# Performance work log

Hardware: AMD Instinct MI355X
Metric: run time of the kernel (lower is better)

## Reference

```python
import jax, jax.numpy as jnp
import numpy as np

N = 50000
E_RAND = 800000
F_IN = 128
H = 4          # num_heads
D_HID = 32     # hidden per-head dim
D_OUT = 32     # output per-head dim
NEG_SLOPE_ATTN = 0.2   # DGL GATConv attention leaky_relu
NEG_SLOPE_ACT = 0.01   # F.leaky_relu default activation


def setup_inputs() -> dict:
    key = jax.random.key(0)
    ks = jax.random.split(key, 12)
    x = jax.random.normal(ks[0], (N, F_IN), dtype=jnp.float32)
    src_r = jax.random.randint(ks[1], (E_RAND,), 0, N, dtype=jnp.int32)
    dst_r = jax.random.randint(ks[2], (E_RAND,), 0, N, dtype=jnp.int32)
    loop = jnp.arange(N, dtype=jnp.int32)
    src = jnp.concatenate([src_r, loop])  # add_self_loop
    dst = jnp.concatenate([dst_r, loop])
    sc1 = 1.0 / np.sqrt(F_IN)
    sc2 = 1.0 / np.sqrt(H * D_HID)
    W1 = jax.random.normal(ks[3], (F_IN, H * D_HID), dtype=jnp.float32) * sc1
    al1 = jax.random.normal(ks[4], (H, D_HID), dtype=jnp.float32) * sc1
    ar1 = jax.random.normal(ks[5], (H, D_HID), dtype=jnp.float32) * sc1
    b1 = jnp.zeros((H * D_HID,), dtype=jnp.float32)
    W2 = jax.random.normal(ks[6], (H * D_HID, H * D_OUT), dtype=jnp.float32) * sc2
    al2 = jax.random.normal(ks[7], (H, D_OUT), dtype=jnp.float32) * sc2
    ar2 = jax.random.normal(ks[8], (H, D_OUT), dtype=jnp.float32) * sc2
    b2 = jnp.zeros((H * D_OUT,), dtype=jnp.float32)
    return {"x": x, "src": src, "dst": dst,
            "W1": W1, "al1": al1, "ar1": ar1, "b1": b1,
            "W2": W2, "al2": al2, "ar2": ar2, "b2": b2}


def gat_conv(x, src, dst, W, al, ar, b, act_slope):
    n = x.shape[0]
    h, d = al.shape
    feat = (x @ W).reshape(n, h, d)                 # [N,H,D]
    el = jnp.einsum('nhd,hd->nh', feat, al)         # [N,H]
    er = jnp.einsum('nhd,hd->nh', feat, ar)
    # edge attention score on edge u->v: leaky_relu(el[u] + er[v])
    e = jax.nn.leaky_relu(el[src] + er[dst], NEG_SLOPE_ATTN)  # [E,H]
    # edge softmax over incoming edges of each dst node (self-loops guarantee >=1 edge)
    m = jax.ops.segment_max(e, dst, num_segments=n)           # [N,H]
    ex = jnp.exp(e - m[dst])
    s = jax.ops.segment_sum(ex, dst, num_segments=n)
    a = ex / s[dst]                                           # [E,H]
    # attention-weighted scatter-sum of source features
    out = jax.ops.segment_sum(a[:, :, None] * feat[src], dst, num_segments=n)  # [N,H,D]
    out = out + b.reshape(h, d)
    if act_slope is not None:
        out = jax.nn.leaky_relu(out, act_slope)
    return out.reshape(n, h * d)                    # flatten(1)


def reference(x, src, dst, W1, al1, ar1, b1, W2, al2, ar2, b2):
    h = gat_conv(x, src, dst, W1, al1, ar1, b1, NEG_SLOPE_ACT)
    out = gat_conv(h, src, dst, W2, al2, ar2, b2, None)  # last layer: no activation
    return out
```

## Files before the change

### kernel.cpp

```cpp
#include <hip/hip_runtime.h>
#include <hip/hip_bf16.h>
#include <hip/hip_fp16.h>

#define HEADS 4
#define DHEAD 32
#define FDIM 128
#define BCAP 64

__global__ __launch_bounds__(256) void k_gemm(
    const float* __restrict__ X, const float* __restrict__ W,
    const float* __restrict__ al, const float* __restrict__ ar,
    __half* __restrict__ feat, float* __restrict__ el, float* __restrict__ er, int n,
    const int* __restrict__ esrc, const int* __restrict__ edst,
    int* __restrict__ deg, int* __restrict__ bucket, int E) {
    __shared__ float Wl[FDIM * FDIM];
    {
        const float4* W4 = (const float4*)W;
        float4* Wl4 = (float4*)Wl;
        for (int i = threadIdx.x; i < FDIM * FDIM / 4; i += 256) Wl4[i] = W4[i];
    }

    if (E > 0) {
        int nb = gridDim.x;
        int echunk = (E + nb - 1) / nb;
        int e0 = blockIdx.x * echunk;
        int e1 = e0 + echunk; if (e1 > E) e1 = E;
        for (int base = e0 + threadIdx.x; base < e1; base += 256 * 8) {
            int d[8], s[8];
#pragma unroll
            for (int j = 0; j < 8; j++) {
                int idx = base + j * 256;
                if (idx < e1) { d[j] = edst[idx]; s[j] = esrc[idx]; }
                else d[j] = -1;
            }
#pragma unroll
            for (int j = 0; j < 8; j++) {
                if (d[j] >= 0) {
                    int p = atomicAdd(&deg[d[j]], 1);
                    if (p < BCAP) bucket[((size_t)d[j] << 6) + p] = s[j];
                }
            }
        }
    }
    __syncthreads();

    int h = __builtin_amdgcn_readfirstlane(threadIdx.x >> 6);
    int lane = threadIdx.x & 63;
    int rb = blockIdx.x * 256 + lane * 4;

    bool v[4];
    const float4* xp[4];
#pragma unroll
    for (int i = 0; i < 4; i++) {
        v[i] = (rb + i) < n;
        int cr = v[i] ? (rb + i) : (n - 1);
        xp[i] = (const float4*)(X + (size_t)cr * FDIM);
    }

    float acc[4][32];
#pragma unroll
    for (int i = 0; i < 4; i++)
#pragma unroll
        for (int j = 0; j < 32; j++) acc[i][j] = 0.f;

    const float* wbase = Wl + h * DHEAD;

    for (int k4 = 0; k4 < FDIM / 4; k4++) {
        float4 a[4];
#pragma unroll
        for (int i = 0; i < 4; i++) a[i] = xp[i][k4];
#pragma unroll
        for (int kk = 0; kk < 4; kk++) {
            const float4* wr = (const float4*)(wbase + (k4 * 4 + kk) * FDIM);
            float s[4];
#pragma unroll
            for (int i = 0; i < 4; i++) s[i] = (&a[i].x)[kk];
#pragma unroll
            for (int j4 = 0; j4 < 8; j4++) {
                float4 wv = wr[j4];
#pragma unroll
                for (int i = 0; i < 4; i++) {
                    acc[i][j4*4+0] += s[i] * wv.x;
                    acc[i][j4*4+1] += s[i] * wv.y;
                    acc[i][j4*4+2] += s[i] * wv.z;
                    acc[i][j4*4+3] += s[i] * wv.w;
                }
            }
        }
    }

    float elv[4], erv[4];
#pragma unroll
    for (int i = 0; i < 4; i++) { elv[i] = 0.f; erv[i] = 0.f; }
#pragma unroll
    for (int j = 0; j < 32; j++) {
        float va = al[h * DHEAD + j], vr = ar[h * DHEAD + j];
#pragma unroll
        for (int i = 0; i < 4; i++) {
            elv[i] += acc[i][j] * va;
            erv[i] += acc[i][j] * vr;
        }
    }
#pragma unroll
    for (int i = 0; i < 4; i++) {
        if (v[i]) {
            el[(size_t)(rb + i) * HEADS + h] = elv[i];
            er[(size_t)(rb + i) * HEADS + h] = erv[i];
        }
    }

#pragma unroll
    for (int i = 0; i < 4; i++) {
        if (!v[i]) continue;
        union { __half2 h2[16]; uint4 u4[4]; } pk;
#pragma unroll
        for (int m = 0; m < 16; m++)
            pk.h2[m] = __floats2half2_rn(acc[i][2*m], acc[i][2*m+1]);
        uint4* dstp = (uint4*)(feat + (size_t)(rb + i) * FDIM + h * DHEAD);
#pragma unroll
        for (int t = 0; t < 4; t++) dstp[t] = pk.u4[t];
    }
}

__global__ __launch_bounds__(256) void k_aggregate(
    const int* __restrict__ bucket, const int* __restrict__ deg,
    const __half2* __restrict__ feat2h, const float* __restrict__ el,
    const float* __restrict__ er, const float* __restrict__ b,
    float* __restrict__ out, int n, int apply_act) {
    int wave = threadIdx.x >> 6;
    int node = blockIdx.x * 4 + wave;
    if (node >= n) return;
    node = __builtin_amdgcn_readfirstlane(node);
    int lane = threadIdx.x & 63;
    int h = lane >> 4;

    float ern = er[(size_t)node * HEADS + h];
    int cnt = __builtin_amdgcn_readfirstlane(deg[node]);
    const int* bkt = bucket + ((size_t)node << 6);

    float ax = 0.f, ay = 0.f, sw = 0.f;
    int i = 0;

    for (; i + 8 <= cnt; i += 8) {
        int s[8];
#pragma unroll
        for (int j = 0; j < 8; j++) s[j] = bkt[i + j];
        float e[8];
#pragma unroll
        for (int j = 0; j < 8; j++) e[j] = el[(size_t)s[j] * HEADS + h];
        __half2 f[8];
#pragma unroll
        for (int j = 0; j < 8; j++) f[j] = feat2h[(size_t)s[j] * 64 + lane];
#pragma unroll
        for (int j = 0; j < 8; j++) {
            float ev = e[j] + ern;
            ev = ev > 0.f ? ev : 0.2f * ev;
            float w = __expf(ev);
            float2 fv = __half22float2(f[j]);
            sw += w; ax += w * fv.x; ay += w * fv.y;
        }
    }
    for (; i + 2 <= cnt; i += 2) {
        int s0 = bkt[i], s1 = bkt[i + 1];
        float e0 = el[(size_t)s0 * HEADS + h];
        float e1 = el[(size_t)s1 * HEADS + h];
        __half2 f0 = feat2h[(size_t)s0 * 64 + lane];
        __half2 f1 = feat2h[(size_t)s1 * 64 + lane];
        e0 += ern; e0 = e0 > 0.f ? e0 : 0.2f * e0;
        e1 += ern; e1 = e1 > 0.f ? e1 : 0.2f * e1;
        float w0 = __expf(e0), w1 = __expf(e1);
        float2 fv0 = __half22float2(f0), fv1 = __half22float2(f1);
        sw += w0 + w1;
        ax += w0 * fv0.x + w1 * fv1.x;
        ay += w0 * fv0.y + w1 * fv1.y;
    }
    if (i < cnt) {
        int s0 = bkt[i];
        float e0 = el[(size_t)s0 * HEADS + h] + ern;
        e0 = e0 > 0.f ? e0 : 0.2f * e0;
        float w0 = __expf(e0);
        float2 fv0 = __half22float2(feat2h[(size_t)s0 * 64 + lane]);
        sw += w0; ax += w0 * fv0.x; ay += w0 * fv0.y;
    }

    float inv = 1.0f / sw;
    float2 bv = ((const float2*)b)[lane];
    float ox = ax * inv + bv.x;
    float oy = ay * inv + bv.y;
    if (apply_act) {
        ox = ox > 0.f ? ox : 0.01f * ox;
        oy = oy > 0.f ? oy : 0.01f * oy;
    }
    float2 o; o.x = ox; o.y = oy;
    ((float2*)out)[(size_t)node * 64 + lane] = o;
}


extern "C" void kernel_launch(void* const* d_in, const int* in_sizes, int n_in,
                              void* d_out, int out_size, void* d_ws, size_t ws_size,
                              hipStream_t stream) {
    const float* x   = (const float*)d_in[0];
    const int*   src = (const int*)d_in[1];
    const int*   dst = (const int*)d_in[2];
    const float* W1  = (const float*)d_in[3];
    const float* al1 = (const float*)d_in[4];
    const float* ar1 = (const float*)d_in[5];
    const float* b1  = (const float*)d_in[6];
    const float* W2  = (const float*)d_in[7];
    const float* al2 = (const float*)d_in[8];
    const float* ar2 = (const float*)d_in[9];
    const float* b2  = (const float*)d_in[10];
    int N = in_sizes[0] / FDIM;
    int E = in_sizes[1];
    float* out = (float*)d_out;

    __half* featA = (__half*)d_ws;
    float* elb    = (float*)(featA + (size_t)N * FDIM);
    float* erb    = elb + (size_t)N * HEADS;
    int*   deg    = (int*)(erb + (size_t)N * HEADS);
    int*   bucket = deg + N;
    float* hbuf   = out;

    int gblocks = (N + 255) / 256;

    hipMemsetAsync(deg, 0, (size_t)N * sizeof(int), stream);

    k_gemm<<<gblocks, 256, 0, stream>>>(x, W1, al1, ar1, featA, elb, erb, N,
                                        src, dst, deg, bucket, E);
    k_aggregate<<<(N + 3) / 4, 256, 0, stream>>>(bucket, deg, (const __half2*)featA,
                                                 elb, erb, b1, hbuf, N, 1);

    k_gemm<<<gblocks, 256, 0, stream>>>(hbuf, W2, al2, ar2, featA, elb, erb, N,
                                        nullptr, nullptr, nullptr, nullptr, 0);
    k_aggregate<<<(N + 3) / 4, 256, 0, stream>>>(bucket, deg, (const __half2*)featA,
                                                 elb, erb, b2, out, N, 0);
}
```

Baseline: 274.6 us.

## Split GEMM grid across heads with per-head W slice and one row per thread

The projection kernel now launches a 2D grid with one block column per head. Each block stages only that head's 128x32 slice of W in shared memory (16 KB instead of 64 KB), and each thread computes one row instead of four. The goal is more blocks and more resident waves per CU, with lower LDS and register pressure and a prefetch of the next X float4. The cost is that each X row is now read four times (once per head), and W loads from shared memory are reused across fewer rows. Edge bucketing runs only in the head-0 blocks.

```diff
diff --git a/kernel.cpp b/kernel.cpp
--- a/kernel.cpp
+++ b/kernel.cpp
@@ -13,14 +13,10 @@
     __half* __restrict__ feat, float* __restrict__ el, float* __restrict__ er, int n,
     const int* __restrict__ esrc, const int* __restrict__ edst,
     int* __restrict__ deg, int* __restrict__ bucket, int E) {
-    __shared__ float Wl[FDIM * FDIM];
-    {
-        const float4* W4 = (const float4*)W;
-        float4* Wl4 = (float4*)Wl;
-        for (int i = threadIdx.x; i < FDIM * FDIM / 4; i += 256) Wl4[i] = W4[i];
-    }
-
-    if (E > 0) {
+    __shared__ float Wl[FDIM * DHEAD];
+    int head = blockIdx.y;
+
+    if (E > 0 && head == 0) {
         int nb = gridDim.x;
         int echunk = (E + nb - 1) / nb;
         int e0 = blockIdx.x * echunk;
@@ -42,81 +38,63 @@
             }
         }
     }
+
+    {
+        float4* Wl4 = (float4*)Wl;
+        for (int i = threadIdx.x; i < FDIM * DHEAD / 4; i += 256) {
+            int k = i >> 3, j4 = i & 7;
+            Wl4[i] = ((const float4*)(W + (size_t)k * FDIM + head * DHEAD))[j4];
+        }
+    }
     __syncthreads();
 
-    int h = __builtin_amdgcn_readfirstlane(threadIdx.x >> 6);
+    int wave = threadIdx.x >> 6;
     int lane = threadIdx.x & 63;
-    int rb = blockIdx.x * 256 + lane * 4;
-
-    bool v[4];
-    const float4* xp[4];
-#pragma unroll
-    for (int i = 0; i < 4; i++) {
-        v[i] = (rb + i) < n;
-        int cr = v[i] ? (rb + i) : (n - 1);
-        xp[i] = (const float4*)(X + (size_t)cr * FDIM);
-    }
-
-    float acc[4][32];
-#pragma unroll
-    for (int i = 0; i < 4; i++)
-#pragma unroll
-        for (int j = 0; j < 32; j++) acc[i][j] = 0.f;
-
-    const float* wbase = Wl + h * DHEAD;
-
+    int row = blockIdx.x * 256 + wave * 64 + lane;
+    bool valid = row < n;
+    int cr = valid ? row : (n - 1);
+    const float4* xp = (const float4*)(X + (size_t)cr * FDIM);
+
+    float acc[32];
+#pragma unroll
+    for (int j = 0; j < 32; j++) acc[j] = 0.f;
+
+    float4 a = xp[0];
     for (int k4 = 0; k4 < FDIM / 4; k4++) {
-        float4 a[4];
-#pragma unroll
-        for (int i = 0; i < 4; i++) a[i] = xp[i][k4];
+        float4 an = (k4 < FDIM / 4 - 1) ? xp[k4 + 1] : a;
 #pragma unroll
         for (int kk = 0; kk < 4; kk++) {
-            const float4* wr = (const float4*)(wbase + (k4 * 4 + kk) * FDIM);
-            float s[4];
-#pragma unroll
-            for (int i = 0; i < 4; i++) s[i] = (&a[i].x)[kk];
+            const float4* wr = (const float4*)(Wl + (k4 * 4 + kk) * DHEAD);
+            float s = (&a.x)[kk];
 #pragma unroll
             for (int j4 = 0; j4 < 8; j4++) {
                 float4 wv = wr[j4];
-#pragma unroll
-                for (int i = 0; i < 4; i++) {
-                    acc[i][j4*4+0] += s[i] * wv.x;
-                    acc[i][j4*4+1] += s[i] * wv.y;
-                    acc[i][j4*4+2] += s[i] * wv.z;
-                    acc[i][j4*4+3] += s[i] * wv.w;
-                }
+                acc[j4 * 4 + 0] += s * wv.x;
+                acc[j4 * 4 + 1] += s * wv.y;
+                acc[j4 * 4 + 2] += s * wv.z;
+                acc[j4 * 4 + 3] += s * wv.w;
             }
         }
-    }
-
-    float elv[4], erv[4];
-#pragma unroll
-    for (int i = 0; i < 4; i++) { elv[i] = 0.f; erv[i] = 0.f; }
+        a = an;
+    }
+
+    float elv = 0.f, erv = 0.f;
 #pragma unroll
     for (int j = 0; j < 32; j++) {
-        float va = al[h * DHEAD + j], vr = ar[h * DHEAD + j];
-#pragma unroll
-        for (int i = 0; i < 4; i++) {
-            elv[i] += acc[i][j] * va;
-            erv[i] += acc[i][j] * vr;
-        }
-    }
-#pragma unroll
-    for (int i = 0; i < 4; i++) {
-        if (v[i]) {
-            el[(size_t)(rb + i) * HEADS + h] = elv[i];
-            er[(size_t)(rb + i) * HEADS + h] = erv[i];
-        }
-    }
-
-#pragma unroll
-    for (int i = 0; i < 4; i++) {
-        if (!v[i]) continue;
+        elv += acc[j] * al[head * DHEAD + j];
+        erv += acc[j] * ar[head * DHEAD + j];
+    }
+    if (valid) {
+        el[(size_t)row * HEADS + head] = elv;
+        er[(size_t)row * HEADS + head] = erv;
+    }
+
+    if (valid) {
         union { __half2 h2[16]; uint4 u4[4]; } pk;
 #pragma unroll
         for (int m = 0; m < 16; m++)
-            pk.h2[m] = __floats2half2_rn(acc[i][2*m], acc[i][2*m+1]);
-        uint4* dstp = (uint4*)(feat + (size_t)(rb + i) * FDIM + h * DHEAD);
+            pk.h2[m] = __floats2half2_rn(acc[2 * m], acc[2 * m + 1]);
+        uint4* dstp = (uint4*)(feat + (size_t)row * FDIM + head * DHEAD);
 #pragma unroll
         for (int t = 0; t < 4; t++) dstp[t] = pk.u4[t];
     }
@@ -221,17 +199,18 @@
     int*   bucket = deg + N;
     float* hbuf   = out;
 
-    int gblocks = (N + 255) / 256;
+    int gx = (N + 255) / 256;
+    dim3 ggrid(gx, HEADS);
 
     hipMemsetAsync(deg, 0, (size_t)N * sizeof(int), stream);
 
-    k_gemm<<<gblocks, 256, 0, stream>>>(x, W1, al1, ar1, featA, elb, erb, N,
-                                        src, dst, deg, bucket, E);
+    k_gemm<<<ggrid, 256, 0, stream>>>(x, W1, al1, ar1, featA, elb, erb, N,
+                                      src, dst, deg, bucket, E);
     k_aggregate<<<(N + 3) / 4, 256, 0, stream>>>(bucket, deg, (const __half2*)featA,
                                                  elb, erb, b1, hbuf, N, 1);
 
-    k_gemm<<<gblocks, 256, 0, stream>>>(hbuf, W2, al2, ar2, featA, elb, erb, N,
-                                        nullptr, nullptr, nullptr, nullptr, 0);
+    k_gemm<<<ggrid, 256, 0, stream>>>(hbuf, W2, al2, ar2, featA, elb, erb, N,
+                                      nullptr, nullptr, nullptr, nullptr, 0);
     k_aggregate<<<(N + 3) / 4, 256, 0, stream>>>(bucket, deg, (const __half2*)featA,
                                                  elb, erb, b2, out, N, 0);
 }
```

Result: slower. 298.2 us (+8.6%).
